# Kernel optimization log

Hardware: AMD Instinct MI355X
Metric: run time of the kernel (lower is better)

## Reference

```python
import math
import jax, jax.numpy as jnp
import numpy as np

HID = 2048      # hidden_size
NH = 16         # num_heads
KD = HID // NH  # key head dim = 128 (even, required by XPOS)
VD = HID        # value_dim (value_factor=1)
VHD = VD // NH  # value head dim
SCALE_BASE = 512
ROPE_BASE = 10000.0
GN_EPS = 1e-5


def _rotate_every_two(x):
    x1 = x[..., ::2]
    x2 = x[..., 1::2]
    return jnp.stack((-x2, x1), axis=-1).reshape(x.shape)


def _dup(a):  # repeat_interleave(x, 2, dim=-1)
    return jnp.repeat(a, 2, axis=-1)


def _xpos_apply(x, pos, inv_freq, xpos_scale, downscale):
    # x: [B, H, S, KD], pos: [B, S]
    posf = pos.astype(jnp.float32)
    angles = posf[:, :, None] * inv_freq[None, None, :]          # [B, S, KD/2]
    sin = _dup(jnp.sin(angles))[:, None]                          # [B, 1, S, KD]
    cos = _dup(jnp.cos(angles))[:, None]
    scale = xpos_scale[None, None, :] ** (posf[:, :, None] / SCALE_BASE)
    if downscale:
        scale = 1.0 / scale
    scale = _dup(scale)[:, None]                                  # [B, 1, S, KD]
    return (x * cos + _rotate_every_two(x) * sin) * scale


def setup_inputs() -> dict:
    key = jax.random.key(0)
    ks = jax.random.split(key, 6)
    B, S = 1, 2048
    std = 1.0 / HID
    x = jax.random.normal(ks[0], (B, S, HID), dtype=jnp.float32)
    position_ids = jnp.broadcast_to(jnp.arange(S, dtype=jnp.int64), (B, S))
    Wq = jax.random.normal(ks[1], (HID, HID), dtype=jnp.float32) * std
    Wk = jax.random.normal(ks[2], (HID, HID), dtype=jnp.float32) * std
    Wv = jax.random.normal(ks[3], (HID, VD), dtype=jnp.float32) * std
    Wg = jax.random.normal(ks[4], (HID, VD), dtype=jnp.float32) * std
    Wo = jax.random.normal(ks[5], (VD, HID), dtype=jnp.float32) * std
    gn_weight = jnp.ones((VD,), dtype=jnp.float32)
    gn_bias = jnp.zeros((VD,), dtype=jnp.float32)
    return {"x": x, "position_ids": position_ids, "Wq": Wq, "Wk": Wk,
            "Wv": Wv, "Wg": Wg, "Wo": Wo,
            "gn_weight": gn_weight, "gn_bias": gn_bias}


def reference(x, position_ids, Wq, Wk, Wv, Wg, Wo, gn_weight, gn_bias):
    B, S, _ = x.shape
    # XPOS / multiscale-decay buffers (deterministic, as in XPOSRelativePosition)
    inv_freq = 1.0 / (ROPE_BASE ** (jnp.arange(0, KD, 2, dtype=jnp.float32) / KD))
    xpos_scale = (jnp.arange(0, KD, 2, dtype=jnp.float32) + 0.4 * KD) / (1.4 * KD)
    gamma = 1.0 - jnp.exp(jnp.linspace(math.log(1.0 / 32), math.log(1.0 / 512), NH))
    log_gamma = jnp.log(gamma)                                    # [NH]

    # projections -> [B, H, S, d]
    q = (x @ Wq).reshape(B, S, NH, KD).transpose(0, 2, 1, 3)
    k = (x @ Wk).reshape(B, S, NH, KD).transpose(0, 2, 1, 3)
    v = (x @ Wv).reshape(B, S, NH, VHD).transpose(0, 2, 1, 3)
    g = x @ Wg                                                    # [B, S, VD]

    q = _xpos_apply(q, position_ids, inv_freq, xpos_scale, downscale=False)
    k = _xpos_apply(k, position_ids, inv_freq, xpos_scale, downscale=True)

    # decay mask: exp(log_gamma * (i-j)) for i>=j else 0   [B, H, S, S]
    relpos = position_ids[:, :, None] - position_ids[:, None, :]  # [B, S, S]
    decay = jnp.exp(log_gamma[None, :, None, None]
                    * jnp.maximum(relpos, 0)[:, None].astype(jnp.float32))
    decay = decay * (relpos >= 0)[:, None].astype(jnp.float32)

    scores = jnp.einsum('bhqd,bhkd->bhqk', q, k) * decay          # [B, H, S, S]
    retained = jnp.einsum('bhqk,bhkv->bhqv', scores, v)           # [B, H, S, VHD]

    # GroupNorm(num_heads, value_dim): normalize each head group per token
    r = retained.transpose(0, 2, 1, 3)                            # [B, S, H, VHD]
    mean = r.mean(axis=-1, keepdims=True)
    var = r.var(axis=-1, keepdims=True)
    rn = (r - mean) * jax.lax.rsqrt(var + GN_EPS)
    rn = rn * gn_weight.reshape(NH, VHD) + gn_bias.reshape(NH, VHD)
    rn = rn.reshape(B, S, VD)

    out = (jax.nn.silu(g) * rn) @ Wo                              # [B, S, HID]
    return out
```

## Files before the change

kernel.cpp:

```cpp
#include <hip/hip_runtime.h>
#include <math.h>

#define S_LEN 2048
#define HIDD  2048
#define NHEAD 16
#define HD    128

#define TILE_SH 4096

typedef __attribute__((ext_vector_type(8))) short short8;
typedef __attribute__((ext_vector_type(4))) float float4v;
typedef unsigned short ushort_t;

static __device__ __forceinline__ ushort_t f2bf(float f) {
    unsigned int u = __float_as_uint(f);
    u += 0x7fff + ((u >> 16) & 1);
    return (ushort_t)(u >> 16);
}
static __device__ __forceinline__ float bf2f(ushort_t s) {
    return __uint_as_float(((unsigned int)s) << 16);
}
__device__ __forceinline__ float silu_f(float x) { return x / (1.f + expf(-x)); }

__device__ __forceinline__ void gl_lds16(const ushort_t* g, short* l) {
    __builtin_amdgcn_global_load_lds((const __attribute__((address_space(1))) void*)g,
                                     (__attribute__((address_space(3))) void*)l, 16, 0, 0);
}

__global__ __launch_bounds__(256)
void split_kernel(const float* __restrict__ in, ushort_t* __restrict__ hi,
                  ushort_t* __restrict__ lo, int n4)
{
    const int i = blockIdx.x * 256 + threadIdx.x;
    if (i >= n4) return;
    const float4 v = ((const float4*)in)[i];
    ushort4 h, l;
    h.x = f2bf(v.x); l.x = f2bf(v.x - bf2f(h.x));
    h.y = f2bf(v.y); l.y = f2bf(v.y - bf2f(h.y));
    h.z = f2bf(v.z); l.z = f2bf(v.z - bf2f(h.z));
    h.w = f2bf(v.w); l.w = f2bf(v.w - bf2f(h.w));
    const int row = i >> 9, c4 = (i & 511) * 4;
    const size_t off = ((size_t)((row >> 7) * 64 + (c4 >> 5))) * TILE_SH
                     + (row & 127) * 32 + (c4 & 31);
    *(ushort4*)&hi[off] = h;
    *(ushort4*)&lo[off] = l;
}

__global__ __launch_bounds__(256)
void addp_kernel(float* __restrict__ out, const float* __restrict__ p, int n4)
{
    const int i = blockIdx.x * 256 + threadIdx.x;
    if (i >= n4) return;
    float4 a = ((const float4*)out)[i];
    const float4 b0 = ((const float4*)p)[i];
    const float4 b1 = ((const float4*)p)[i + n4];
    const float4 b2 = ((const float4*)p)[i + 2 * n4];
    a.x += b0.x + b1.x + b2.x;
    a.y += b0.y + b1.y + b2.y;
    a.z += b0.z + b1.z + b2.z;
    a.w += b0.w + b1.w + b2.w;
    ((float4*)out)[i] = a;
}

__global__ __launch_bounds__(256)
void split_transpose(const float* __restrict__ W, ushort_t* __restrict__ Thi,
                     ushort_t* __restrict__ Tlo)
{
    __shared__ float t[64][65];
    const int k0 = blockIdx.y * 64, n0 = blockIdx.x * 64;
    const int tx = threadIdx.x & 15, ty = threadIdx.x >> 4;
    #pragma unroll
    for (int it = 0; it < 4; it++) {
        const int k = ty + it * 16;
        const float4 v = *(const float4*)&W[(size_t)(k0 + k) * HIDD + n0 + tx * 4];
        t[k][tx * 4 + 0] = v.x; t[k][tx * 4 + 1] = v.y;
        t[k][tx * 4 + 2] = v.z; t[k][tx * 4 + 3] = v.w;
    }
    __syncthreads();
    #pragma unroll
    for (int it = 0; it < 4; it++) {
        const int n = ty + it * 16;
        ushort4 h, l; float a;
        a = t[tx * 4 + 0][n]; h.x = f2bf(a); l.x = f2bf(a - bf2f(h.x));
        a = t[tx * 4 + 1][n]; h.y = f2bf(a); l.y = f2bf(a - bf2f(h.y));
        a = t[tx * 4 + 2][n]; h.z = f2bf(a); l.z = f2bf(a - bf2f(h.z));
        a = t[tx * 4 + 3][n]; h.w = f2bf(a); l.w = f2bf(a - bf2f(h.w));
        const int nn_ = n0 + n, kk_ = k0 + tx * 4;
        const size_t off = ((size_t)((nn_ >> 7) * 64 + (kk_ >> 5))) * TILE_SH
                         + (nn_ & 127) * 32 + (kk_ & 31);
        *(ushort4*)&Thi[off] = h;
        *(ushort4*)&Tlo[off] = l;
    }
}

template<int MODE>
__global__ __launch_bounds__(256, 2)
void mfma_gemm(const ushort_t* __restrict__ Ahi, const ushort_t* __restrict__ Alo,
               const ushort_t* __restrict__ WT, const int* __restrict__ pos_ids,
               ushort_t* __restrict__ qhi, ushort_t* __restrict__ qlo,
               ushort_t* __restrict__ khi, ushort_t* __restrict__ klo,
               ushort_t* __restrict__ vThi, ushort_t* __restrict__ vTlo,
               float* __restrict__ gbuf, float* __restrict__ outC)
{
    __shared__ __align__(16) short sm[40960];

    const int tid = threadIdx.x;
    const int w = tid >> 6, L = tid & 63;
    const int qd = L >> 4, lc = L & 15;
    const int lin = blockIdx.x;
    int n0, m0, kh = 0;
    if (MODE == 0) {
        n0 = (((lin & 7) << 2) + ((lin >> 3) & 3)) << 8;
        m0 = (lin >> 5) << 7;
    } else {
        n0 = (lin & 7) << 8;
        m0 = ((lin >> 3) & 15) << 7;
        kh = lin >> 7;
    }
    const size_t PL = (size_t)HIDD * HIDD;

    int sel, nn;
    const ushort_t *Bhi, *Blo;
    if (MODE == 0) {
        sel = n0 >> 11; nn = n0 & 2047;
        Bhi = WT + (size_t)sel * 2 * PL; Blo = Bhi + PL;
    } else {
        sel = -1; nn = n0;
        Bhi = WT; Blo = WT + PL;
    }

    const ushort_t* pbase = (w == 0) ? Ahi : (w == 1) ? Alo : (w == 2) ? Bhi : Blo;
    const int rt = ((w < 2) ? m0 : nn) >> 7;
    const ushort_t* tb0 = pbase + (size_t)rt * 64 * TILE_SH + L * 8;

    const int wm = (w & 1) * 64;
    const int wnh = w >> 1;
    int aoff[4], boff[8];
    #pragma unroll
    for (int i = 0; i < 4; i++) aoff[i] = (wm + i * 16 + lc) * 32 + qd * 8;
    #pragma unroll
    for (int jj = 0; jj < 8; jj++) boff[jj] = (jj * 16 + lc) * 32 + qd * 8;

    float4v acc[4][8];
    #pragma unroll
    for (int i = 0; i < 4; i++)
        #pragma unroll
        for (int jj = 0; jj < 8; jj++)
            #pragma unroll
            for (int r = 0; r < 4; r++) acc[i][jj][r] = 0.f;

    const int kt0 = (MODE == 1) ? kh * 16 : 0;
    const int kt1 = (MODE == 1) ? kt0 + 16 : 64;

    {
        const ushort_t* g = tb0 + (size_t)kt0 * TILE_SH;
        if (w < 2) {
            short* d = sm + w * 4096;
            #pragma unroll
            for (int t = 0; t < 8; t++) gl_lds16(g + t * 512, d + t * 512);
        } else {
            short* d = sm + 8192 + (w - 2) * 8192;
            #pragma unroll
            for (int t = 0; t < 8; t++) gl_lds16(g + t * 512, d + t * 512);
            #pragma unroll
            for (int t = 0; t < 8; t++) gl_lds16(g + 64 * TILE_SH + t * 512, d + 4096 + t * 512);
        }
        asm volatile("s_waitcnt vmcnt(0)" ::: "memory");
        __builtin_amdgcn_s_barrier();
        __builtin_amdgcn_sched_barrier(0);
    }

    int cur = 0;
    for (int kt = kt0; kt < kt1; kt++) {
        if (w >= 2 && kt + 1 < kt1) {
            const ushort_t* g = tb0 + (size_t)(kt + 1) * TILE_SH;
            short* d = sm + 8192 + ((cur ^ 1) * 16384) + (w - 2) * 8192;
            #pragma unroll
            for (int t = 0; t < 8; t++) gl_lds16(g + t * 512, d + t * 512);
            #pragma unroll
            for (int t = 0; t < 8; t++) gl_lds16(g + 64 * TILE_SH + t * 512, d + 4096 + t * 512);
        }

        short8 ah[4], al[4];
        #pragma unroll
        for (int i = 0; i < 4; i++) {
            ah[i] = *(const short8*)(sm + aoff[i]);
            al[i] = *(const short8*)(sm + 4096 + aoff[i]);
        }
        const short* bb = sm + 8192 + cur * 16384 + wnh * 4096;
        #pragma unroll
        for (int jh = 0; jh < 2; jh++) {
            short8 bh[4], bl[4];
            #pragma unroll
            for (int j = 0; j < 4; j++) {
                bh[j] = *(const short8*)(bb + boff[jh * 4 + j]);
                bl[j] = *(const short8*)(bb + 8192 + boff[jh * 4 + j]);
            }
            #pragma unroll
            for (int i = 0; i < 4; i++)
                #pragma unroll
                for (int j = 0; j < 4; j++) {
                    acc[i][jh * 4 + j] = __builtin_amdgcn_mfma_f32_16x16x32_bf16(ah[i], bh[j], acc[i][jh * 4 + j], 0, 0, 0);
                    acc[i][jh * 4 + j] = __builtin_amdgcn_mfma_f32_16x16x32_bf16(al[i], bh[j], acc[i][jh * 4 + j], 0, 0, 0);
                    acc[i][jh * 4 + j] = __builtin_amdgcn_mfma_f32_16x16x32_bf16(ah[i], bl[j], acc[i][jh * 4 + j], 0, 0, 0);
                }
        }

        asm volatile("s_waitcnt lgkmcnt(0)" ::: "memory");
        __builtin_amdgcn_s_barrier();
        __builtin_amdgcn_sched_barrier(0);
        if (w < 2 && kt + 1 < kt1) {
            const ushort_t* g = tb0 + (size_t)(kt + 1) * TILE_SH;
            short* d = sm + w * 4096;
            #pragma unroll
            for (int t = 0; t < 8; t++) gl_lds16(g + t * 512, d + t * 512);
        }
        asm volatile("s_waitcnt vmcnt(0)" ::: "memory");
        __builtin_amdgcn_s_barrier();
        __builtin_amdgcn_sched_barrier(0);
        cur ^= 1;
    }

    float* ob = (float*)sm;
    const int mh = w & 1;
    const int headb = nn >> 7;

    #pragma unroll
    for (int i = 0; i < 4; i++) {
        #pragma unroll
        for (int jj = 0; jj < 8; jj++)
            #pragma unroll
            for (int r = 0; r < 4; r++)
                ob[(mh * 16 + qd * 4 + r) * 260 + wnh * 128 + jj * 16 + lc] = acc[i][jj][r];
        __syncthreads();

        if (MODE == 1 || sel == 3) {
            float* dst = (MODE == 1) ? ((kh == 0) ? outC : gbuf + (size_t)(kh - 1) * PL)
                                     : gbuf;
            #pragma unroll
            for (int p = 0; p < 8; p++) {
                const int row = p * 4 + (tid >> 6);
                const int c = (tid & 63) * 4;
                const int grow = m0 + (row >> 4) * 64 + i * 16 + (row & 15);
                const float4 vv = *(const float4*)&ob[row * 260 + c];
                *(float4*)&dst[(size_t)grow * HIDD + nn + c] = vv;
            }
        } else if (sel == 2) {
            const int d = tid >> 1, hs = tid & 1;
            const int sbase = m0 + hs * 64 + i * 16;
            #pragma unroll
            for (int nh = 0; nh < 2; nh++) {
                short8 h0, h1, l0, l1;
                #pragma unroll
                for (int sp = 0; sp < 8; sp++) {
                    float a = ob[(hs * 16 + sp) * 260 + nh * 128 + d];
                    ushort_t hb = f2bf(a);
                    h0[sp] = (short)hb; l0[sp] = (short)f2bf(a - bf2f(hb));
                    a = ob[(hs * 16 + 8 + sp) * 260 + nh * 128 + d];
                    hb = f2bf(a);
                    h1[sp] = (short)hb; l1[sp] = (short)f2bf(a - bf2f(hb));
                }
                ushort_t* dh = vThi + ((size_t)(headb + nh) * HD + d) * S_LEN + sbase;
                ushort_t* dl = vTlo + ((size_t)(headb + nh) * HD + d) * S_LEN + sbase;
                *(short8*)dh = h0; *(short8*)(dh + 8) = h1;
                *(short8*)dl = l0; *(short8*)(dl + 8) = l1;
            }
        } else {
            const float sgn = (sel == 0) ? 1.f : -1.f;
            ushort_t* dhb = (sel == 0) ? qhi : khi;
            ushort_t* dlb = (sel == 0) ? qlo : klo;
            #pragma unroll
            for (int nh = 0; nh < 2; nh++) {
                const int head = headb + nh;
                #pragma unroll
                for (int p = 0; p < 2; p++) {
                    const int row = p * 16 + (tid >> 4);
                    const int c8 = (tid & 15) * 8;
                    const int grow = m0 + (row >> 4) * 64 + i * 16 + (row & 15);
                    const float pos = (float)pos_ids[grow];
                    const float pe = sgn * pos * (1.f / 512.f);
                    short8 hv, lv;
                    #pragma unroll
                    for (int pp = 0; pp < 4; pp++) {
                        const int d = c8 + pp * 2;
                        const float v0 = ob[row * 260 + nh * 128 + d];
                        const float v1 = ob[row * 260 + nh * 128 + d + 1];
                        const float invf = exp2f(-(float)d * (13.28771238f / 128.f));
                        float s, c_; sincosf(pos * invf, &s, &c_);
                        const float scl = exp2f(log2f(((float)d + 51.2f) * (1.f / 179.2f)) * pe);
                        const float e0 = (v0 * c_ - v1 * s) * scl;
                        const float e1 = (v1 * c_ + v0 * s) * scl;
                        const ushort_t h0 = f2bf(e0), h1 = f2bf(e1);
                        hv[pp * 2] = (short)h0;  hv[pp * 2 + 1] = (short)h1;
                        lv[pp * 2] = (short)f2bf(e0 - bf2f(h0));
                        lv[pp * 2 + 1] = (short)f2bf(e1 - bf2f(h1));
                    }
                    *(short8*)&dhb[((size_t)head * S_LEN + grow) * HD + c8] = hv;
                    *(short8*)&dlb[((size_t)head * S_LEN + grow) * HD + c8] = lv;
                }
            }
        }
        __syncthreads();
    }
}

#define KROW 136
#define VROW 40
#define KH_  0
#define KL_  (32 * KROW)
#define VH_  (2 * 32 * KROW)
#define VL_  (VH_ + 128 * VROW)
#define PH_  (VH_ + 2 * 128 * VROW)
#define PLO_ (PH_ + 64 * VROW)
#define YH_  8704
#define YL_  (YH_ + 64 * KROW)
__global__ __launch_bounds__(256, 2)
void retention2(const ushort_t* __restrict__ qhi, const ushort_t* __restrict__ qlo,
                const ushort_t* __restrict__ khi, const ushort_t* __restrict__ klo,
                const ushort_t* __restrict__ vThi, const ushort_t* __restrict__ vTlo,
                const float* __restrict__ gbuf, const float* __restrict__ gnw,
                const float* __restrict__ gnb,
                ushort_t* __restrict__ yhi, ushort_t* __restrict__ ylo)
{
    __shared__ __align__(16) short sm[26112];

    const int h = blockIdx.y;
    const int qb = (gridDim.x - 1) - blockIdx.x;
    const int r0 = qb * 64;
    const int tid = threadIdx.x;
    const int w = tid >> 6, L = tid & 63;
    const int qd = L >> 4, lc = L & 15;

    const float e = -3.4657359f + (float)h * ((-6.2383246f + 3.4657359f) / 15.f);
    const float lg2g = logf(1.f - expf(e)) * 1.44269504f;

    short8 qfh[4], qfl[4];
    {
        const size_t qb0 = ((size_t)h * S_LEN + r0 + w * 16 + lc) * HD + qd * 8;
        #pragma unroll
        for (int ks = 0; ks < 4; ks++) {
            qfh[ks] = *(const short8*)(qhi + qb0 + ks * 32);
            qfl[ks] = *(const short8*)(qlo + qb0 + ks * 32);
        }
    }

    float4v osum[2][4];
    #pragma unroll
    for (int mt = 0; mt < 2; mt++)
        #pragma unroll
        for (int j = 0; j < 4; j++)
            #pragma unroll
            for (int r = 0; r < 4; r++) osum[mt][j][r] = 0.f;

    const int qh_ = w >> 1, vh_ = w & 1;
    const int nch = (r0 + 64) / 32;

    for (int ch = 0; ch < nch; ch++) {
        const int kg0 = ch * 32;
        #pragma unroll
        for (int t = 0; t < 4; t++) {
            const int c = t * 256 + tid;
            const int p = c >> 9, r = (c >> 4) & 31, qq = c & 15;
            const ushort_t* src = (p ? klo : khi) + ((size_t)h * S_LEN + kg0 + r) * HD + qq * 8;
            *(short8*)(sm + (p ? KL_ : KH_) + r * KROW + qq * 8) = *(const short8*)src;
        }
        #pragma unroll
        for (int t = 0; t < 4; t++) {
            const int c = t * 256 + tid;
            const int p = c >> 9, r = (c >> 2) & 127, qq = c & 3;
            const ushort_t* src = (p ? vTlo : vThi) + ((size_t)h * HD + r) * S_LEN + kg0 + qq * 8;
            *(short8*)(sm + (p ? VL_ : VH_) + r * VROW + qq * 8) = *(const short8*)src;
        }
        __syncthreads();

        float4v sacc[2];
        #pragma unroll
        for (int j = 0; j < 2; j++)
            #pragma unroll
            for (int r = 0; r < 4; r++) sacc[j][r] = 0.f;
        #pragma unroll
        for (int ks = 0; ks < 4; ks++) {
            #pragma unroll
            for (int j = 0; j < 2; j++) {
                const short8 bh = *(const short8*)(sm + KH_ + (j * 16 + lc) * KROW + ks * 32 + qd * 8);
                const short8 bl = *(const short8*)(sm + KL_ + (j * 16 + lc) * KROW + ks * 32 + qd * 8);
                sacc[j] = __builtin_amdgcn_mfma_f32_16x16x32_bf16(qfh[ks], bh, sacc[j], 0, 0, 0);
                sacc[j] = __builtin_amdgcn_mfma_f32_16x16x32_bf16(qfl[ks], bh, sacc[j], 0, 0, 0);
                sacc[j] = __builtin_amdgcn_mfma_f32_16x16x32_bf16(qfh[ks], bl, sacc[j], 0, 0, 0);
            }
        }
        #pragma unroll
        for (int j = 0; j < 2; j++)
            #pragma unroll
            for (int r = 0; r < 4; r++) {
                const int dq = (r0 + w * 16 + qd * 4 + r) - (kg0 + j * 16 + lc);
                const float p = (dq >= 0) ? sacc[j][r] * exp2f(lg2g * (float)dq) : 0.f;
                const ushort_t hb = f2bf(p);
                const int off = (w * 16 + qd * 4 + r) * VROW + j * 16 + lc;
                sm[PH_ + off]  = (short)hb;
                sm[PLO_ + off] = (short)f2bf(p - bf2f(hb));
            }
        __syncthreads();

        #pragma unroll
        for (int mt = 0; mt < 2; mt++) {
            const short8 pfh = *(const short8*)(sm + PH_  + (qh_ * 32 + mt * 16 + lc) * VROW + qd * 8);
            const short8 pfl = *(const short8*)(sm + PLO_ + (qh_ * 32 + mt * 16 + lc) * VROW + qd * 8);
            #pragma unroll
            for (int j = 0; j < 4; j++) {
                const short8 vfh = *(const short8*)(sm + VH_ + (vh_ * 64 + j * 16 + lc) * VROW + qd * 8);
                const short8 vfl = *(const short8*)(sm + VL_ + (vh_ * 64 + j * 16 + lc) * VROW + qd * 8);
                osum[mt][j] = __builtin_amdgcn_mfma_f32_16x16x32_bf16(pfh, vfh, osum[mt][j], 0, 0, 0);
                osum[mt][j] = __builtin_amdgcn_mfma_f32_16x16x32_bf16(pfl, vfh, osum[mt][j], 0, 0, 0);
                osum[mt][j] = __builtin_amdgcn_mfma_f32_16x16x32_bf16(pfh, vfl, osum[mt][j], 0, 0, 0);
            }
        }
        __syncthreads();
    }

    float* fr = (float*)sm;
    #pragma unroll
    for (int mt = 0; mt < 2; mt++)
        #pragma unroll
        for (int r = 0; r < 4; r++) {
            float s1 = 0.f, s2 = 0.f;
            #pragma unroll
            for (int j = 0; j < 4; j++) { const float v = osum[mt][j][r]; s1 += v; s2 += v * v; }
            const int row = qh_ * 32 + mt * 16 + qd * 4 + r;
            fr[row * 32 + vh_ * 16 + lc] = s1;
            fr[2048 + row * 32 + vh_ * 16 + lc] = s2;
        }
    __syncthreads();
    if (tid < 64) {
        float s1 = 0.f, s2 = 0.f;
        #pragma unroll
        for (int t = 0; t < 32; t++) { s1 += fr[tid * 32 + t]; s2 += fr[2048 + tid * 32 + t]; }
        const float mean = s1 * (1.f / 128.f);
        const float var  = s2 * (1.f / 128.f) - mean * mean;
        fr[4096 + tid] = mean;
        fr[4160 + tid] = 1.f / sqrtf(var + 1e-5f);
    }
    __syncthreads();

    #pragma unroll
    for (int mt = 0; mt < 2; mt++)
        #pragma unroll
        for (int r = 0; r < 4; r++) {
            const int row = qh_ * 32 + mt * 16 + qd * 4 + r;
            const float mean = fr[4096 + row], inv = fr[4160 + row];
            const int grow = r0 + row;
            #pragma unroll
            for (int j = 0; j < 4; j++) {
                const int col = vh_ * 64 + j * 16 + lc;
                const float gv = gbuf[(size_t)grow * HIDD + h * HD + col];
                const float o = ((osum[mt][j][r] - mean) * inv * gnw[h * HD + col]
                                 + gnb[h * HD + col]) * silu_f(gv);
                const ushort_t hb = f2bf(o);
                sm[YH_ + row * KROW + col] = (short)hb;
                sm[YL_ + row * KROW + col] = (short)f2bf(o - bf2f(hb));
            }
        }
    __syncthreads();
    {
        const int r_ = tid >> 2, cs = (tid & 3) * 32;
        const int grow = r0 + r_;
        const size_t tb = ((size_t)((grow >> 7) * 64 + h * 4 + (tid & 3))) * TILE_SH
                        + (grow & 127) * 32;
        #pragma unroll
        for (int c8 = 0; c8 < 4; c8++) {
            *(short8*)(yhi + tb + c8 * 8) = *(const short8*)(sm + YH_ + r_ * KROW + cs + c8 * 8);
            *(short8*)(ylo + tb + c8 * 8) = *(const short8*)(sm + YL_ + r_ * KROW + cs + c8 * 8);
        }
    }
}

extern "C" void kernel_launch(void* const* d_in, const int* in_sizes, int n_in,
                              void* d_out, int out_size, void* d_ws, size_t ws_size,
                              hipStream_t stream) {
    const float* x   = (const float*)d_in[0];
    const int*   pid = (const int*)d_in[1];
    const float* W[5] = {(const float*)d_in[2], (const float*)d_in[3], (const float*)d_in[4],
                         (const float*)d_in[5], (const float*)d_in[6]};
    const float* gnw = (const float*)d_in[7];
    const float* gnb = (const float*)d_in[8];
    float* out = (float*)d_out;
    (void)in_sizes; (void)n_in; (void)out_size; (void)ws_size;

    const size_t PL = (size_t)HIDD * HIDD;

    ushort_t* wt   = (ushort_t*)d_ws;
    ushort_t* xhi  = wt + 10 * PL;
    ushort_t* xlo  = xhi + PL;
    ushort_t* qhi_ = xlo + PL;
    ushort_t* qlo_ = qhi_ + PL;
    ushort_t* khi_ = qlo_ + PL;
    ushort_t* klo_ = khi_ + PL;
    ushort_t* vThi = klo_ + PL;
    ushort_t* vTlo = vThi + PL;
    float*    gbuf = (float*)(vTlo + PL);
    ushort_t* yhi  = (ushort_t*)(gbuf + PL);
    ushort_t* ylo  = yhi + PL;
    float*    pb   = (float*)xhi;

    split_kernel<<<(int)(PL / 4 / 256), 256, 0, stream>>>(x, xhi, xlo, (int)(PL / 4));
    for (int m = 0; m < 5; m++)
        split_transpose<<<dim3(32, 32), 256, 0, stream>>>(W[m], wt + (size_t)m * 2 * PL,
                                                          wt + (size_t)m * 2 * PL + PL);

    mfma_gemm<0><<<512, 256, 0, stream>>>(xhi, xlo, wt, pid,
        qhi_, qlo_, khi_, klo_, vThi, vTlo, gbuf, nullptr);

    retention2<<<dim3(32, 16), 256, 0, stream>>>(qhi_, qlo_, khi_, klo_, vThi, vTlo,
        gbuf, gnw, gnb, yhi, ylo);

    mfma_gemm<1><<<512, 256, 0, stream>>>(yhi, ylo, wt + 8 * PL, pid,
        nullptr, nullptr, nullptr, nullptr, nullptr, nullptr, pb, out);

    addp_kernel<<<(int)(PL / 4 / 256), 256, 0, stream>>>(out, pb, (int)(PL / 4));
}
```

Measured before the change: 579.2 us.

## Split GEMM block across eight waves to halve per-wave accumulator tile

The projection GEMM kernel now launches 512 threads (8 waves) per block instead of 256. Each wave computes a 64x64 output sub-tile instead of 64x128, which halves the accumulator registers and the B fragment loads per wave, and the B-tile global-to-LDS loads are spread over four waves instead of two. The epilogue is reworked so each half of the block handles one head. The aim is more waves in flight per CU to hide LDS and MFMA latency, at the cost of more barrier participants and duplicated A-fragment reads across waves.

```diff
diff --git a/kernel.cpp b/kernel.cpp
--- a/kernel.cpp
+++ b/kernel.cpp
@@ -94,7 +94,7 @@
 }
 
 template<int MODE>
-__global__ __launch_bounds__(256, 2)
+__global__ __launch_bounds__(512, 4)
 void mfma_gemm(const ushort_t* __restrict__ Ahi, const ushort_t* __restrict__ Alo,
                const ushort_t* __restrict__ WT, const int* __restrict__ pos_ids,
                ushort_t* __restrict__ qhi, ushort_t* __restrict__ qlo,
@@ -129,25 +129,27 @@
         Bhi = WT; Blo = WT + PL;
     }
 
-    const ushort_t* pbase = (w == 0) ? Ahi : (w == 1) ? Alo : (w == 2) ? Bhi : Blo;
-    const int rt = ((w < 2) ? m0 : nn) >> 7;
+    const ushort_t* pbase = (w == 0) ? Ahi : (w == 1) ? Alo : (w < 4) ? Bhi : Blo;
+    const int rt = (w < 2) ? (m0 >> 7) : ((nn >> 7) + ((w - 2) & 1));
     const ushort_t* tb0 = pbase + (size_t)rt * 64 * TILE_SH + L * 8;
 
     const int wm = (w & 1) * 64;
-    const int wnh = w >> 1;
-    int aoff[4], boff[8];
+    const int ns = w >> 1;
+    const int bt = ns >> 1;
+    const int br = (ns & 1) * 64;
+    int aoff[4], boff[4];
     #pragma unroll
     for (int i = 0; i < 4; i++) aoff[i] = (wm + i * 16 + lc) * 32 + qd * 8;
     #pragma unroll
-    for (int jj = 0; jj < 8; jj++) boff[jj] = (jj * 16 + lc) * 32 + qd * 8;
-
-    float4v acc[4][8];
+    for (int j = 0; j < 4; j++) boff[j] = bt * 4096 + (br + j * 16 + lc) * 32 + qd * 8;
+
+    float4v acc[4][4];
     #pragma unroll
     for (int i = 0; i < 4; i++)
         #pragma unroll
-        for (int jj = 0; jj < 8; jj++)
-            #pragma unroll
-            for (int r = 0; r < 4; r++) acc[i][jj][r] = 0.f;
+        for (int j = 0; j < 4; j++)
+            #pragma unroll
+            for (int r = 0; r < 4; r++) acc[i][j][r] = 0.f;
 
     const int kt0 = (MODE == 1) ? kh * 16 : 0;
     const int kt1 = (MODE == 1) ? kt0 + 16 : 64;
@@ -158,12 +160,10 @@
             short* d = sm + w * 4096;
             #pragma unroll
             for (int t = 0; t < 8; t++) gl_lds16(g + t * 512, d + t * 512);
-        } else {
-            short* d = sm + 8192 + (w - 2) * 8192;
+        } else if (w < 6) {
+            short* d = sm + 8192 + (w - 2) * 4096;
             #pragma unroll
             for (int t = 0; t < 8; t++) gl_lds16(g + t * 512, d + t * 512);
-            #pragma unroll
-            for (int t = 0; t < 8; t++) gl_lds16(g + 64 * TILE_SH + t * 512, d + 4096 + t * 512);
         }
         asm volatile("s_waitcnt vmcnt(0)" ::: "memory");
         __builtin_amdgcn_s_barrier();
@@ -172,39 +172,33 @@
 
     int cur = 0;
     for (int kt = kt0; kt < kt1; kt++) {
-        if (w >= 2 && kt + 1 < kt1) {
+        if (w >= 2 && w < 6 && kt + 1 < kt1) {
             const ushort_t* g = tb0 + (size_t)(kt + 1) * TILE_SH;
-            short* d = sm + 8192 + ((cur ^ 1) * 16384) + (w - 2) * 8192;
+            short* d = sm + 8192 + (cur ^ 1) * 16384 + (w - 2) * 4096;
             #pragma unroll
             for (int t = 0; t < 8; t++) gl_lds16(g + t * 512, d + t * 512);
-            #pragma unroll
-            for (int t = 0; t < 8; t++) gl_lds16(g + 64 * TILE_SH + t * 512, d + 4096 + t * 512);
-        }
-
-        short8 ah[4], al[4];
+        }
+
+        short8 ah[4], al[4], bh[4], bl[4];
+        const short* bb = sm + 8192 + cur * 16384;
         #pragma unroll
         for (int i = 0; i < 4; i++) {
             ah[i] = *(const short8*)(sm + aoff[i]);
             al[i] = *(const short8*)(sm + 4096 + aoff[i]);
         }
-        const short* bb = sm + 8192 + cur * 16384 + wnh * 4096;
-        #pragma unroll
-        for (int jh = 0; jh < 2; jh++) {
-            short8 bh[4], bl[4];
+        #pragma unroll
+        for (int j = 0; j < 4; j++) {
+            bh[j] = *(const short8*)(bb + boff[j]);
+            bl[j] = *(const short8*)(bb + 8192 + boff[j]);
+        }
+        #pragma unroll
+        for (int i = 0; i < 4; i++)
             #pragma unroll
             for (int j = 0; j < 4; j++) {
-                bh[j] = *(const short8*)(bb + boff[jh * 4 + j]);
-                bl[j] = *(const short8*)(bb + 8192 + boff[jh * 4 + j]);
-            }
-            #pragma unroll
-            for (int i = 0; i < 4; i++)
-                #pragma unroll
-                for (int j = 0; j < 4; j++) {
-                    acc[i][jh * 4 + j] = __builtin_amdgcn_mfma_f32_16x16x32_bf16(ah[i], bh[j], acc[i][jh * 4 + j], 0, 0, 0);
-                    acc[i][jh * 4 + j] = __builtin_amdgcn_mfma_f32_16x16x32_bf16(al[i], bh[j], acc[i][jh * 4 + j], 0, 0, 0);
-                    acc[i][jh * 4 + j] = __builtin_amdgcn_mfma_f32_16x16x32_bf16(ah[i], bl[j], acc[i][jh * 4 + j], 0, 0, 0);
-                }
-        }
+                acc[i][j] = __builtin_amdgcn_mfma_f32_16x16x32_bf16(ah[i], bh[j], acc[i][j], 0, 0, 0);
+                acc[i][j] = __builtin_amdgcn_mfma_f32_16x16x32_bf16(al[i], bh[j], acc[i][j], 0, 0, 0);
+                acc[i][j] = __builtin_amdgcn_mfma_f32_16x16x32_bf16(ah[i], bl[j], acc[i][j], 0, 0, 0);
+            }
 
         asm volatile("s_waitcnt lgkmcnt(0)" ::: "memory");
         __builtin_amdgcn_s_barrier();
@@ -228,76 +222,72 @@
     #pragma unroll
     for (int i = 0; i < 4; i++) {
         #pragma unroll
-        for (int jj = 0; jj < 8; jj++)
+        for (int j = 0; j < 4; j++)
             #pragma unroll
             for (int r = 0; r < 4; r++)
-                ob[(mh * 16 + qd * 4 + r) * 260 + wnh * 128 + jj * 16 + lc] = acc[i][jj][r];
+                ob[(mh * 16 + qd * 4 + r) * 260 + ns * 64 + j * 16 + lc] = acc[i][j][r];
         __syncthreads();
 
         if (MODE == 1 || sel == 3) {
             float* dst = (MODE == 1) ? ((kh == 0) ? outC : gbuf + (size_t)(kh - 1) * PL)
                                      : gbuf;
             #pragma unroll
-            for (int p = 0; p < 8; p++) {
-                const int row = p * 4 + (tid >> 6);
+            for (int p = 0; p < 4; p++) {
+                const int row = p * 8 + (tid >> 6);
                 const int c = (tid & 63) * 4;
                 const int grow = m0 + (row >> 4) * 64 + i * 16 + (row & 15);
                 const float4 vv = *(const float4*)&ob[row * 260 + c];
                 *(float4*)&dst[(size_t)grow * HIDD + nn + c] = vv;
             }
         } else if (sel == 2) {
-            const int d = tid >> 1, hs = tid & 1;
+            const int nh = tid >> 8, rem = tid & 255;
+            const int d = rem >> 1, hs = rem & 1;
             const int sbase = m0 + hs * 64 + i * 16;
-            #pragma unroll
-            for (int nh = 0; nh < 2; nh++) {
-                short8 h0, h1, l0, l1;
-                #pragma unroll
-                for (int sp = 0; sp < 8; sp++) {
-                    float a = ob[(hs * 16 + sp) * 260 + nh * 128 + d];
-                    ushort_t hb = f2bf(a);
-                    h0[sp] = (short)hb; l0[sp] = (short)f2bf(a - bf2f(hb));
-                    a = ob[(hs * 16 + 8 + sp) * 260 + nh * 128 + d];
-                    hb = f2bf(a);
-                    h1[sp] = (short)hb; l1[sp] = (short)f2bf(a - bf2f(hb));
-                }
-                ushort_t* dh = vThi + ((size_t)(headb + nh) * HD + d) * S_LEN + sbase;
-                ushort_t* dl = vTlo + ((size_t)(headb + nh) * HD + d) * S_LEN + sbase;
-                *(short8*)dh = h0; *(short8*)(dh + 8) = h1;
-                *(short8*)dl = l0; *(short8*)(dl + 8) = l1;
-            }
+            short8 h0, h1, l0, l1;
+            #pragma unroll
+            for (int sp = 0; sp < 8; sp++) {
+                float a = ob[(hs * 16 + sp) * 260 + nh * 128 + d];
+                ushort_t hb = f2bf(a);
+                h0[sp] = (short)hb; l0[sp] = (short)f2bf(a - bf2f(hb));
+                a = ob[(hs * 16 + 8 + sp) * 260 + nh * 128 + d];
+                hb = f2bf(a);
+                h1[sp] = (short)hb; l1[sp] = (short)f2bf(a - bf2f(hb));
+            }
+            ushort_t* dh = vThi + ((size_t)(headb + nh) * HD + d) * S_LEN + sbase;
+            ushort_t* dl = vTlo + ((size_t)(headb + nh) * HD + d) * S_LEN + sbase;
+            *(short8*)dh = h0; *(short8*)(dh + 8) = h1;
+            *(short8*)dl = l0; *(short8*)(dl + 8) = l1;
         } else {
             const float sgn = (sel == 0) ? 1.f : -1.f;
             ushort_t* dhb = (sel == 0) ? qhi : khi;
             ushort_t* dlb = (sel == 0) ? qlo : klo;
-            #pragma unroll
-            for (int nh = 0; nh < 2; nh++) {
-                const int head = headb + nh;
+            const int nh = tid >> 8, rem = tid & 255;
+            const int head = headb + nh;
+            #pragma unroll
+            for (int p = 0; p < 2; p++) {
+                const int row = p * 16 + (rem >> 4);
+                const int c8 = (rem & 15) * 8;
+                const int grow = m0 + (row >> 4) * 64 + i * 16 + (row & 15);
+                const float pos = (float)pos_ids[grow];
+                const float pe = sgn * pos * (1.f / 512.f);
+                short8 hv, lv;
                 #pragma unroll
-                for (int p = 0; p < 2; p++) {
-                    const int row = p * 16 + (tid >> 4);
-                    const int c8 = (tid & 15) * 8;
-                    const int grow = m0 + (row >> 4) * 64 + i * 16 + (row & 15);
-                    const float pos = (float)pos_ids[grow];
-                    const float pe = sgn * pos * (1.f / 512.f);
-                    short8 hv, lv;
-                    #pragma unroll
-                    for (int pp = 0; pp < 4; pp++) {
-                        const int d = c8 + pp * 2;
-                        const float v0 = ob[row * 260 + nh * 128 + d];
-                        const float v1 = ob[row * 260 + nh * 128 + d + 1];
-                        const float invf = exp2f(-(float)d * (13.28771238f / 128.f));
-                        float s, c_; sincosf(pos * invf, &s, &c_);
-                        const float scl = exp2f(log2f(((float)d + 51.2f) * (1.f / 179.2f)) * pe);
-                        const float e0 = (v0 * c_ - v1 * s) * scl;
-                        const float e1 = (v1 * c_ + v0 * s) * scl;
-                        const ushort_t h0 = f2bf(e0), h1 = f2bf(e1);
-                        hv[pp * 2] = (short)h0;  hv[pp * 2 + 1] = (short)h1;
-                        lv[pp * 2] = (short)f2bf(e0 - bf2f(h0));
-                        lv[pp * 2 + 1] = (short)f2bf(e1 - bf2f(h1));
-                    }
-                    *(short8*)&dhb[((size_t)head * S_LEN + grow) * HD + c8] = hv;
-                    *(short8*)&dlb[((size_t)head * S_LEN + grow) * HD + c8] = lv;
+                for (int pp = 0; pp < 4; pp++) {
+                    const int d = c8 + pp * 2;
+                    const float v0 = ob[row * 260 + nh * 128 + d];
+                    const float v1 = ob[row * 260 + nh * 128 + d + 1];
+                    const float invf = exp2f(-(float)d * (13.28771238f / 128.f));
+                    float s, c_; sincosf(pos * invf, &s, &c_);
+                    const float scl = exp2f(log2f(((float)d + 51.2f) * (1.f / 179.2f)) * pe);
+                    const float e0 = (v0 * c_ - v1 * s) * scl;
+                    const float e1 = (v1 * c_ + v0 * s) * scl;
+                    const ushort_t h0 = f2bf(e0), h1 = f2bf(e1);
+                    hv[pp * 2] = (short)h0;  hv[pp * 2 + 1] = (short)h1;
+                    lv[pp * 2] = (short)f2bf(e0 - bf2f(h0));
+                    lv[pp * 2 + 1] = (short)f2bf(e1 - bf2f(h1));
                 }
+                *(short8*)&dhb[((size_t)head * S_LEN + grow) * HD + c8] = hv;
+                *(short8*)&dlb[((size_t)head * S_LEN + grow) * HD + c8] = lv;
             }
         }
         __syncthreads();
@@ -507,13 +497,13 @@
         split_transpose<<<dim3(32, 32), 256, 0, stream>>>(W[m], wt + (size_t)m * 2 * PL,
                                                           wt + (size_t)m * 2 * PL + PL);
 
-    mfma_gemm<0><<<512, 256, 0, stream>>>(xhi, xlo, wt, pid,
+    mfma_gemm<0><<<512, 512, 0, stream>>>(xhi, xlo, wt, pid,
         qhi_, qlo_, khi_, klo_, vThi, vTlo, gbuf, nullptr);
 
     retention2<<<dim3(32, 16), 256, 0, stream>>>(qhi_, qlo_, khi_, klo_, vThi, vTlo,
         gbuf, gnw, gnb, yhi, ylo);
 
-    mfma_gemm<1><<<512, 256, 0, stream>>>(yhi, ylo, wt + 8 * PL, pid,
+    mfma_gemm<1><<<512, 512, 0, stream>>>(yhi, ylo, wt + 8 * PL, pid,
         nullptr, nullptr, nullptr, nullptr, nullptr, nullptr, pb, out);
 
     addp_kernel<<<(int)(PL / 4 / 256), 256, 0, stream>>>(out, pb, (int)(PL / 4));
```

After: 544.6 us. -6.0%, faster.
